# Optimization experiments

Hardware: AMD Instinct MI355X
Metric: run time of the kernel (lower is better)

The kernel has to match this reference:

```python
import jax, jax.numpy as jnp
import numpy as np

B, K, D = 8192, 8192, 512

def setup_inputs() -> dict:
    key = jax.random.key(0)
    k1, k2 = jax.random.split(key)
    z_e = jax.random.normal(k1, (B, D), dtype=jnp.float32)
    # codebook: kaiming-uniform-initialized parameter; random normal scaled similarly is fine for a numeric baseline
    codebook = jax.random.normal(k2, (K, D), dtype=jnp.float32)
    return {"z_e": z_e, "codebook": codebook}

def reference(z_e, codebook):
    # Euclidean distances via dot-product expansion (same math as
    # torch.norm(z_e[:,None]-codebook[None], dim=-1) without the [B,K,D] intermediate):
    # d^2 = ||z||^2 - 2 z.c + ||c||^2
    z_sq = jnp.sum(z_e * z_e, axis=-1, keepdims=True)          # [B,1]
    c_sq = jnp.sum(codebook * codebook, axis=-1)               # [K]
    cross = jnp.einsum('bd,kd->bk', z_e, codebook)             # [B,K] GEMM
    d2 = jnp.maximum(z_sq - 2.0 * cross + c_sq[None, :], 0.0)  # clamp fp negatives
    distances = jnp.sqrt(d2)                                   # [B,K]
    indices = jnp.argmin(distances, axis=-1)                   # [B]
    z_q = jnp.take(codebook, indices, axis=0)                  # [B,D] gather
    return (z_q, indices)
```

## Files before the change

kernel.cpp:

```cpp
#include <hip/hip_runtime.h>


constexpr int Bn = 8192;
constexpr int Kn = 8192;
constexpr int Dn = 512;

#define SLOTS 16

using half8  = __attribute__((ext_vector_type(8)))  _Float16;
using f32x16 = __attribute__((ext_vector_type(16))) float;

#define WS_CSQ  0u
#define WS_PART (32u * 1024u)
#define WS_ZH   (2u * 1024u * 1024u)
#define WS_ZL   (10u * 1024u * 1024u)
#define WS_CH   (18u * 1024u * 1024u)
#define WS_CL   (26u * 1024u * 1024u)

typedef __attribute__((address_space(3))) void       as3_void;
typedef const __attribute__((address_space(1))) void as1_cvoid;


__global__ __launch_bounds__(256) void prep_kernel(const float* __restrict__ Z,
                                                   const float* __restrict__ Cb,
                                                   char* __restrict__ ws) {
  const int gid = blockIdx.x * 256 + threadIdx.x;
  const int mat = gid >> 19;
  const int cid = gid & 524287;
  int row, colf;
  if (mat == 0) {
    const int tile = cid >> 8;
    const int quad = (cid >> 3) & 31;
    const int ch = cid & 7;
    const int x = ch ^ (quad & 7);
    row = (tile >> 5) * 128 + quad * 4 + (x >> 1);
    colf = (tile & 31) * 16 + (x & 1) * 8;
  } else {
    const int tile = cid >> 9;
    const int quad = (cid >> 3) & 63;
    const int ch = cid & 7;
    const int x = ch ^ (quad & 7);
    row = (tile >> 5) * 256 + quad * 4 + (x >> 1);
    colf = (tile & 31) * 16 + (x & 1) * 8;
  }
  const float* src = (mat ? Cb : Z) + (size_t)row * Dn + colf;
  const float4 v0 = *reinterpret_cast<const float4*>(src);
  const float4 v1 = *reinterpret_cast<const float4*>(src + 4);
  const float f[8] = {v0.x, v0.y, v0.z, v0.w, v1.x, v1.y, v1.z, v1.w};
  _Float16 h[8], l[8];
#pragma unroll
  for (int j = 0; j < 8; ++j) {
    h[j] = (_Float16)f[j];
    l[j] = (_Float16)(f[j] - (float)h[j]);
  }
  const half8 vh = {h[0], h[1], h[2], h[3], h[4], h[5], h[6], h[7]};
  const half8 vl = {l[0], l[1], l[2], l[3], l[4], l[5], l[6], l[7]};
  char* hb = ws + (mat ? WS_CH : WS_ZH);
  char* lb = ws + (mat ? WS_CL : WS_ZL);
  *reinterpret_cast<half8*>(hb + (size_t)cid * 16) = vh;
  *reinterpret_cast<half8*>(lb + (size_t)cid * 16) = vl;
}

__global__ __launch_bounds__(256) void csq_kernel(const float* __restrict__ C,
                                                  float* __restrict__ csq) {
  const int wave = threadIdx.x >> 6;
  const int lane = threadIdx.x & 63;
  const int row = blockIdx.x * 4 + wave;
  const float4* p = reinterpret_cast<const float4*>(C + (size_t)row * Dn);
  float s = 0.f;
#pragma unroll
  for (int r = 0; r < 2; ++r) {
    float4 v = p[lane * 2 + r];
    s += v.x * v.x + v.y * v.y + v.z * v.z + v.w * v.w;
  }
#pragma unroll
  for (int off = 32; off; off >>= 1) s += __shfl_xor(s, off);
  if (lane == 0) csq[row] = s;
}

__global__ __launch_bounds__(256, 2) void vq_mfma(const char* __restrict__ ws,
                                                  const float* __restrict__ csq,
                                                  float2* __restrict__ partials) {
  __shared__ uint4 lds4[4608];
  char* lds = (char*)lds4;

  const int t = threadIdx.x;
  const int lane = t & 63;
  const int w = t >> 6;
  const int wm = w >> 1, wn = w & 1;
  const int rowblk = blockIdx.x >> 3;
  const int split = blockIdx.x & 7;
  const int r31 = lane & 31;
  const int kh = lane >> 5;

  int offA[2][2], offB[4][2];
#pragma unroll
  for (int ms = 0; ms < 2; ++ms) {
    const int row = wm * 64 + ms * 32 + r31;
    const int quad = row >> 2;
    const int base = quad * 128 + (((((row & 3) << 1) + kh) ^ (quad & 7)) << 4);
    offA[ms][0] = base;
    offA[ms][1] = 4096 + base;
  }
#pragma unroll
  for (int ns = 0; ns < 4; ++ns) {
    const int row = wn * 128 + ns * 32 + r31;
    const int quad = row >> 2;
    const int base = quad * 128 + (((((row & 3) << 1) + kh) ^ (quad & 7)) << 4);
    offB[ns][0] = 8192 + base;
    offB[ns][1] = 16384 + base;
  }

  const char* ZH = ws + WS_ZH;
  const char* ZL = ws + WS_ZL;
  const char* CH = ws + WS_CH;
  const char* CL = ws + WS_CL;
  const size_t lane16 = (size_t)lane * 16 + (size_t)w * 1024;

  auto STAGE = [&](int u, int bsel) {
    const int kt = u & 31, panel = u >> 5;
    const size_t at = (size_t)(rowblk * 32 + kt) * 4096 + lane16;
    const size_t bt = (size_t)(((split * 4 + panel) * 32) + kt) * 8192 + lane16;
    char* d = lds + bsel * 24576 + w * 1024;
    __builtin_amdgcn_global_load_lds((as1_cvoid*)(ZH + at), (as3_void*)(d), 16, 0, 0);
    __builtin_amdgcn_global_load_lds((as1_cvoid*)(ZL + at), (as3_void*)(d + 4096), 16, 0, 0);
    __builtin_amdgcn_global_load_lds((as1_cvoid*)(CH + bt), (as3_void*)(d + 8192), 16, 0, 0);
    __builtin_amdgcn_global_load_lds((as1_cvoid*)(CH + bt + 4096), (as3_void*)(d + 12288), 16, 0, 0);
    __builtin_amdgcn_global_load_lds((as1_cvoid*)(CL + bt), (as3_void*)(d + 16384), 16, 0, 0);
    __builtin_amdgcn_global_load_lds((as1_cvoid*)(CL + bt + 4096), (as3_void*)(d + 20480), 16, 0, 0);
  };

  float bs[2][16];
  int bidx[2][16];
#pragma unroll
  for (int ms = 0; ms < 2; ++ms)
#pragma unroll
    for (int r = 0; r < 16; ++r) { bs[ms][r] = 1e30f; bidx[ms][r] = 0x7fffffff; }

  STAGE(0, 0);
  STAGE(1, 1);
  asm volatile("s_waitcnt vmcnt(6)" ::: "memory");
  __builtin_amdgcn_s_barrier();

  int cur = 0;
  for (int panel = 0; panel < 4; ++panel) {
    const int n0i = split * 1024 + panel * 256 + wn * 128 + r31;
    float cs[4];
#pragma unroll
    for (int ns = 0; ns < 4; ++ns) cs[ns] = csq[n0i + ns * 32];
    f32x16 acc[2][4] = {};

    for (int kt = 0; kt < 32; ++kt) {
      const int u = panel * 32 + kt;
      const int nx2 = cur >= 1 ? cur - 1 : cur + 2;
      if (u + 2 < 128) STAGE(u + 2, nx2);

      const char* Lb = lds + cur * 24576;
      half8 ah[2], al[2], bh[4], bl[4];
#pragma unroll
      for (int ms = 0; ms < 2; ++ms) {
        ah[ms] = *reinterpret_cast<const half8*>(Lb + offA[ms][0]);
        al[ms] = *reinterpret_cast<const half8*>(Lb + offA[ms][1]);
      }
#pragma unroll
      for (int ns = 0; ns < 4; ++ns) {
        bh[ns] = *reinterpret_cast<const half8*>(Lb + offB[ns][0]);
        bl[ns] = *reinterpret_cast<const half8*>(Lb + offB[ns][1]);
      }
#pragma unroll
      for (int ms = 0; ms < 2; ++ms)
#pragma unroll
        for (int ns = 0; ns < 4; ++ns)
          acc[ms][ns] = __builtin_amdgcn_mfma_f32_32x32x16_f16(
              ah[ms], bh[ns], acc[ms][ns], 0, 0, 0);
#pragma unroll
      for (int ms = 0; ms < 2; ++ms)
#pragma unroll
        for (int ns = 0; ns < 4; ++ns)
          acc[ms][ns] = __builtin_amdgcn_mfma_f32_32x32x16_f16(
              ah[ms], bl[ns], acc[ms][ns], 0, 0, 0);
#pragma unroll
      for (int ms = 0; ms < 2; ++ms)
#pragma unroll
        for (int ns = 0; ns < 4; ++ns)
          acc[ms][ns] = __builtin_amdgcn_mfma_f32_32x32x16_f16(
              al[ms], bh[ns], acc[ms][ns], 0, 0, 0);

      if (u < 126)
        asm volatile("s_waitcnt vmcnt(6) lgkmcnt(0)" ::: "memory");
      else
        asm volatile("s_waitcnt vmcnt(0) lgkmcnt(0)" ::: "memory");
      __builtin_amdgcn_s_barrier();
      cur = cur == 2 ? 0 : cur + 1;
    }

#pragma unroll
    for (int ms = 0; ms < 2; ++ms)
#pragma unroll
      for (int r = 0; r < 16; ++r) {
        float s = cs[0] - 2.f * acc[ms][0][r];
        int ni = n0i;
#pragma unroll
        for (int ns = 1; ns < 4; ++ns) {
          const float s2 = cs[ns] - 2.f * acc[ms][ns][r];
          if (s2 < s) { s = s2; ni = n0i + ns * 32; }
        }
        if (s < bs[ms][r]) { bs[ms][r] = s; bidx[ms][r] = ni; }
      }
  }

  float fs = 1e30f;
  int fi = 0;
#pragma unroll
  for (int ms = 0; ms < 2; ++ms)
#pragma unroll
    for (int r = 0; r < 16; ++r) {
      float s = bs[ms][r];
      int ni = bidx[ms][r];
#pragma unroll
      for (int off = 1; off <= 16; off <<= 1) {
        const float os = __shfl_xor(s, off);
        const int oi = __shfl_xor(ni, off);
        if (os < s || (os == s && oi < ni)) { s = os; ni = oi; }
      }
      if (r31 == ms * 16 + r) { fs = s; fi = ni; }
    }
  const int msL = r31 >> 4;
  const int rL = r31 & 15;
  const int grow = rowblk * 128 + wm * 64 + msL * 32 + (rL & 3) + 8 * (rL >> 2) + 4 * kh;
  partials[grow * SLOTS + split * 2 + wn] = make_float2(fs, (float)fi);
}

__global__ __launch_bounds__(128) void gather_kernel(const float* __restrict__ C,
                                                     const float2* __restrict__ partials,
                                                     float* __restrict__ zq,
                                                     float* __restrict__ idx_out) {
  const int b = blockIdx.x;
  float bsv = 1e30f;
  int bi = 0x7fffffff;
#pragma unroll
  for (int s = 0; s < SLOTS; ++s) {
    const float2 p = partials[b * SLOTS + s];
    const int i = (int)p.y;
    if (p.x < bsv || (p.x == bsv && i < bi)) { bsv = p.x; bi = i; }
  }
  const int t = threadIdx.x;
  const float4 v = *reinterpret_cast<const float4*>(C + (size_t)bi * Dn + t * 4);
  *reinterpret_cast<float4*>(zq + (size_t)b * Dn + t * 4) = v;
  if (t == 0) idx_out[b] = (float)bi;
}

extern "C" void kernel_launch(void* const* d_in, const int* in_sizes, int n_in,
                              void* d_out, int out_size, void* d_ws, size_t ws_size,
                              hipStream_t stream) {
  const float* Z = (const float*)d_in[0];
  const float* C = (const float*)d_in[1];
  float* out = (float*)d_out;

  char* ws = (char*)d_ws;
  float* csq = (float*)(ws + WS_CSQ);
  float2* partials = (float2*)(ws + WS_PART);

  prep_kernel<<<4096, 256, 0, stream>>>(Z, C, ws);
  csq_kernel<<<Kn / 4, 256, 0, stream>>>(C, csq);
  vq_mfma<<<(Bn / 128) * 8, 256, 0, stream>>>(ws, csq, partials);
  gather_kernel<<<Bn, 128, 0, stream>>>(C, partials, out, out + (size_t)Bn * Dn);
}
```

Baseline: 231.5 us.

## Replace LDS-staged GEMM pipeline with direct global-to-register fragment loads

Drops the triple-buffered LDS staging with global_load_lds and barriers. Each wave now loads its MFMA fragments straight from global memory into registers, using a new prep layout that stores the data in MFMA operand order. B fragments are double-buffered in registers, and the per-panel argmin now does the cross-lane shuffle reduction inside each fold. This removes LDS traffic and block barriers, but in exchange every wave fetches A and B directly from L2/global with no sharing of tiles across waves.

```diff
diff --git a/kernel.cpp b/kernel.cpp
--- a/kernel.cpp
+++ b/kernel.cpp
@@ -17,9 +17,6 @@
 #define WS_CH   (18u * 1024u * 1024u)
 #define WS_CL   (26u * 1024u * 1024u)
 
-typedef __attribute__((address_space(3))) void       as3_void;
-typedef const __attribute__((address_space(1))) void as1_cvoid;
-
 
 __global__ __launch_bounds__(256) void prep_kernel(const float* __restrict__ Z,
                                                    const float* __restrict__ Cb,
@@ -27,23 +24,17 @@
   const int gid = blockIdx.x * 256 + threadIdx.x;
   const int mat = gid >> 19;
   const int cid = gid & 524287;
-  int row, colf;
+  int row, col;
   if (mat == 0) {
-    const int tile = cid >> 8;
-    const int quad = (cid >> 3) & 31;
-    const int ch = cid & 7;
-    const int x = ch ^ (quad & 7);
-    row = (tile >> 5) * 128 + quad * 4 + (x >> 1);
-    colf = (tile & 31) * 16 + (x & 1) * 8;
+    const int tile = cid >> 8, c = cid & 255;
+    row = (tile >> 5) * 128 + ((c >> 6) << 5) + (c & 31);
+    col = ((tile & 31) << 4) + (((c >> 5) & 1) << 3);
   } else {
-    const int tile = cid >> 9;
-    const int quad = (cid >> 3) & 63;
-    const int ch = cid & 7;
-    const int x = ch ^ (quad & 7);
-    row = (tile >> 5) * 256 + quad * 4 + (x >> 1);
-    colf = (tile & 31) * 16 + (x & 1) * 8;
-  }
-  const float* src = (mat ? Cb : Z) + (size_t)row * Dn + colf;
+    const int tile = cid >> 9, c = cid & 511;
+    row = (tile >> 5) * 256 + ((c >> 6) << 5) + (c & 31);
+    col = ((tile & 31) << 4) + (((c >> 5) & 1) << 3);
+  }
+  const float* src = (mat ? Cb : Z) + (size_t)row * Dn + col;
   const float4 v0 = *reinterpret_cast<const float4*>(src);
   const float4 v1 = *reinterpret_cast<const float4*>(src + 4);
   const float f[8] = {v0.x, v0.y, v0.z, v0.w, v1.x, v1.y, v1.z, v1.w};
@@ -81,9 +72,6 @@
 __global__ __launch_bounds__(256, 2) void vq_mfma(const char* __restrict__ ws,
                                                   const float* __restrict__ csq,
                                                   float2* __restrict__ partials) {
-  __shared__ uint4 lds4[4608];
-  char* lds = (char*)lds4;
-
   const int t = threadIdx.x;
   const int lane = t & 63;
   const int w = t >> 6;
@@ -93,142 +81,120 @@
   const int r31 = lane & 31;
   const int kh = lane >> 5;
 
-  int offA[2][2], offB[4][2];
-#pragma unroll
-  for (int ms = 0; ms < 2; ++ms) {
-    const int row = wm * 64 + ms * 32 + r31;
-    const int quad = row >> 2;
-    const int base = quad * 128 + (((((row & 3) << 1) + kh) ^ (quad & 7)) << 4);
-    offA[ms][0] = base;
-    offA[ms][1] = 4096 + base;
-  }
-#pragma unroll
-  for (int ns = 0; ns < 4; ++ns) {
-    const int row = wn * 128 + ns * 32 + r31;
-    const int quad = row >> 2;
-    const int base = quad * 128 + (((((row & 3) << 1) + kh) ^ (quad & 7)) << 4);
-    offB[ns][0] = 8192 + base;
-    offB[ns][1] = 16384 + base;
-  }
-
   const char* ZH = ws + WS_ZH;
   const char* ZL = ws + WS_ZL;
   const char* CH = ws + WS_CH;
   const char* CL = ws + WS_CL;
-  const size_t lane16 = (size_t)lane * 16 + (size_t)w * 1024;
-
-  auto STAGE = [&](int u, int bsel) {
-    const int kt = u & 31, panel = u >> 5;
-    const size_t at = (size_t)(rowblk * 32 + kt) * 4096 + lane16;
-    const size_t bt = (size_t)(((split * 4 + panel) * 32) + kt) * 8192 + lane16;
-    char* d = lds + bsel * 24576 + w * 1024;
-    __builtin_amdgcn_global_load_lds((as1_cvoid*)(ZH + at), (as3_void*)(d), 16, 0, 0);
-    __builtin_amdgcn_global_load_lds((as1_cvoid*)(ZL + at), (as3_void*)(d + 4096), 16, 0, 0);
-    __builtin_amdgcn_global_load_lds((as1_cvoid*)(CH + bt), (as3_void*)(d + 8192), 16, 0, 0);
-    __builtin_amdgcn_global_load_lds((as1_cvoid*)(CH + bt + 4096), (as3_void*)(d + 12288), 16, 0, 0);
-    __builtin_amdgcn_global_load_lds((as1_cvoid*)(CL + bt), (as3_void*)(d + 16384), 16, 0, 0);
-    __builtin_amdgcn_global_load_lds((as1_cvoid*)(CL + bt + 4096), (as3_void*)(d + 20480), 16, 0, 0);
+
+  const size_t abase = (size_t)rowblk * 32 * 4096 + (size_t)(wm * 2) * 1024 + lane * 16;
+  const size_t bbase = (size_t)(wn * 4) * 1024 + lane * 16;
+
+  float cs[16];
+#pragma unroll
+  for (int p = 0; p < 4; ++p)
+#pragma unroll
+    for (int ns = 0; ns < 4; ++ns)
+      cs[p * 4 + ns] = csq[split * 1024 + p * 256 + wn * 128 + ns * 32 + r31];
+
+  float rs = 1e30f;
+  int ri = 0x7fffffff;
+  f32x16 acc[2][4] = {};
+  half8 b0h[4], b0l[4], b1h[4], b1l[4];
+
+  {
+    const size_t bt = (size_t)(split * 128) * 8192 + bbase;
+#pragma unroll
+    for (int ns = 0; ns < 4; ++ns) {
+      b0h[ns] = *reinterpret_cast<const half8*>(CH + bt + ns * 1024);
+      b0l[ns] = *reinterpret_cast<const half8*>(CL + bt + ns * 1024);
+    }
+  }
+
+  auto step = [&](int u, half8 (&BH)[4], half8 (&BL)[4],
+                  half8 (&NH)[4], half8 (&NL)[4]) {
+    if (u + 1 < 128) {
+      const size_t bt = (size_t)(split * 128 + u + 1) * 8192 + bbase;
+#pragma unroll
+      for (int ns = 0; ns < 4; ++ns) {
+        NH[ns] = *reinterpret_cast<const half8*>(CH + bt + ns * 1024);
+        NL[ns] = *reinterpret_cast<const half8*>(CL + bt + ns * 1024);
+      }
+    }
+    const size_t at = (size_t)(u & 31) * 4096 + abase;
+    half8 ah[2], al[2];
+#pragma unroll
+    for (int ms = 0; ms < 2; ++ms) {
+      ah[ms] = *reinterpret_cast<const half8*>(ZH + at + ms * 1024);
+      al[ms] = *reinterpret_cast<const half8*>(ZL + at + ms * 1024);
+    }
+#pragma unroll
+    for (int ms = 0; ms < 2; ++ms)
+#pragma unroll
+      for (int ns = 0; ns < 4; ++ns)
+        acc[ms][ns] = __builtin_amdgcn_mfma_f32_32x32x16_f16(
+            ah[ms], BH[ns], acc[ms][ns], 0, 0, 0);
+#pragma unroll
+    for (int ms = 0; ms < 2; ++ms)
+#pragma unroll
+      for (int ns = 0; ns < 4; ++ns)
+        acc[ms][ns] = __builtin_amdgcn_mfma_f32_32x32x16_f16(
+            ah[ms], BL[ns], acc[ms][ns], 0, 0, 0);
+#pragma unroll
+    for (int ms = 0; ms < 2; ++ms)
+#pragma unroll
+      for (int ns = 0; ns < 4; ++ns)
+        acc[ms][ns] = __builtin_amdgcn_mfma_f32_32x32x16_f16(
+            al[ms], BH[ns], acc[ms][ns], 0, 0, 0);
   };
 
-  float bs[2][16];
-  int bidx[2][16];
-#pragma unroll
-  for (int ms = 0; ms < 2; ++ms)
-#pragma unroll
-    for (int r = 0; r < 16; ++r) { bs[ms][r] = 1e30f; bidx[ms][r] = 0x7fffffff; }
-
-  STAGE(0, 0);
-  STAGE(1, 1);
-  asm volatile("s_waitcnt vmcnt(6)" ::: "memory");
-  __builtin_amdgcn_s_barrier();
-
-  int cur = 0;
-  for (int panel = 0; panel < 4; ++panel) {
-    const int n0i = split * 1024 + panel * 256 + wn * 128 + r31;
-    float cs[4];
-#pragma unroll
-    for (int ns = 0; ns < 4; ++ns) cs[ns] = csq[n0i + ns * 32];
-    f32x16 acc[2][4] = {};
-
-    for (int kt = 0; kt < 32; ++kt) {
-      const int u = panel * 32 + kt;
-      const int nx2 = cur >= 1 ? cur - 1 : cur + 2;
-      if (u + 2 < 128) STAGE(u + 2, nx2);
-
-      const char* Lb = lds + cur * 24576;
-      half8 ah[2], al[2], bh[4], bl[4];
-#pragma unroll
-      for (int ms = 0; ms < 2; ++ms) {
-        ah[ms] = *reinterpret_cast<const half8*>(Lb + offA[ms][0]);
-        al[ms] = *reinterpret_cast<const half8*>(Lb + offA[ms][1]);
+  auto fold = [&](float c0, float c1, float c2, float c3, int pbase) {
+    const int nlane = pbase + wn * 128 + r31;
+#pragma unroll
+    for (int ms = 0; ms < 2; ++ms)
+#pragma unroll
+      for (int r = 0; r < 16; ++r) {
+        float s = c0 - 2.f * acc[ms][0][r];
+        int ni = nlane;
+        const float s1 = c1 - 2.f * acc[ms][1][r];
+        if (s1 < s) { s = s1; ni = nlane + 32; }
+        const float s2 = c2 - 2.f * acc[ms][2][r];
+        if (s2 < s) { s = s2; ni = nlane + 64; }
+        const float s3 = c3 - 2.f * acc[ms][3][r];
+        if (s3 < s) { s = s3; ni = nlane + 96; }
+#pragma unroll
+        for (int off = 1; off <= 16; off <<= 1) {
+          const float os = __shfl_xor(s, off);
+          const int oi = __shfl_xor(ni, off);
+          if (os < s || (os == s && oi < ni)) { s = os; ni = oi; }
+        }
+        if (r31 == ms * 16 + r) {
+          if (s < rs || (s == rs && ni < ri)) { rs = s; ri = ni; }
+        }
       }
 #pragma unroll
-      for (int ns = 0; ns < 4; ++ns) {
-        bh[ns] = *reinterpret_cast<const half8*>(Lb + offB[ns][0]);
-        bl[ns] = *reinterpret_cast<const half8*>(Lb + offB[ns][1]);
+    for (int ms = 0; ms < 2; ++ms)
+#pragma unroll
+      for (int ns = 0; ns < 4; ++ns) acc[ms][ns] = (f32x16)0.f;
+  };
+
+  for (int up = 0; up < 64; ++up) {
+    step(2 * up, b0h, b0l, b1h, b1l);
+    step(2 * up + 1, b1h, b1l, b0h, b0l);
+    if ((up & 15) == 15) {
+      const int pbase = split * 1024 + (up >> 4) * 256;
+      switch (up >> 4) {
+        case 0: fold(cs[0], cs[1], cs[2], cs[3], pbase); break;
+        case 1: fold(cs[4], cs[5], cs[6], cs[7], pbase); break;
+        case 2: fold(cs[8], cs[9], cs[10], cs[11], pbase); break;
+        default: fold(cs[12], cs[13], cs[14], cs[15], pbase); break;
       }
-#pragma unroll
-      for (int ms = 0; ms < 2; ++ms)
-#pragma unroll
-        for (int ns = 0; ns < 4; ++ns)
-          acc[ms][ns] = __builtin_amdgcn_mfma_f32_32x32x16_f16(
-              ah[ms], bh[ns], acc[ms][ns], 0, 0, 0);
-#pragma unroll
-      for (int ms = 0; ms < 2; ++ms)
-#pragma unroll
-        for (int ns = 0; ns < 4; ++ns)
-          acc[ms][ns] = __builtin_amdgcn_mfma_f32_32x32x16_f16(
-              ah[ms], bl[ns], acc[ms][ns], 0, 0, 0);
-#pragma unroll
-      for (int ms = 0; ms < 2; ++ms)
-#pragma unroll
-        for (int ns = 0; ns < 4; ++ns)
-          acc[ms][ns] = __builtin_amdgcn_mfma_f32_32x32x16_f16(
-              al[ms], bh[ns], acc[ms][ns], 0, 0, 0);
-
-      if (u < 126)
-        asm volatile("s_waitcnt vmcnt(6) lgkmcnt(0)" ::: "memory");
-      else
-        asm volatile("s_waitcnt vmcnt(0) lgkmcnt(0)" ::: "memory");
-      __builtin_amdgcn_s_barrier();
-      cur = cur == 2 ? 0 : cur + 1;
-    }
-
-#pragma unroll
-    for (int ms = 0; ms < 2; ++ms)
-#pragma unroll
-      for (int r = 0; r < 16; ++r) {
-        float s = cs[0] - 2.f * acc[ms][0][r];
-        int ni = n0i;
-#pragma unroll
-        for (int ns = 1; ns < 4; ++ns) {
-          const float s2 = cs[ns] - 2.f * acc[ms][ns][r];
-          if (s2 < s) { s = s2; ni = n0i + ns * 32; }
-        }
-        if (s < bs[ms][r]) { bs[ms][r] = s; bidx[ms][r] = ni; }
-      }
-  }
-
-  float fs = 1e30f;
-  int fi = 0;
-#pragma unroll
-  for (int ms = 0; ms < 2; ++ms)
-#pragma unroll
-    for (int r = 0; r < 16; ++r) {
-      float s = bs[ms][r];
-      int ni = bidx[ms][r];
-#pragma unroll
-      for (int off = 1; off <= 16; off <<= 1) {
-        const float os = __shfl_xor(s, off);
-        const int oi = __shfl_xor(ni, off);
-        if (os < s || (os == s && oi < ni)) { s = os; ni = oi; }
-      }
-      if (r31 == ms * 16 + r) { fs = s; fi = ni; }
-    }
+    }
+  }
+
   const int msL = r31 >> 4;
   const int rL = r31 & 15;
   const int grow = rowblk * 128 + wm * 64 + msL * 32 + (rL & 3) + 8 * (rL >> 2) + 4 * kh;
-  partials[grow * SLOTS + split * 2 + wn] = make_float2(fs, (float)fi);
+  partials[grow * SLOTS + split * 2 + wn] = make_float2(rs, (float)ri);
 }
 
 __global__ __launch_bounds__(128) void gather_kernel(const float* __restrict__ C,
```

Measured after the change: 273.2 us. 1.18x slower.
